# Optimization experiments

Measured on AMD Instinct MI355X. Metric: run time of the kernel, lower is better.

Reference implementation:

```python
import jax, jax.numpy as jnp
import numpy as np
import math

DN = ('NCHW', 'OIHW', 'NCHW')

def conv2d(x, w, b=None, pad=0):
    y = jax.lax.conv_general_dilated(x, w, (1, 1), [(pad, pad), (pad, pad)], dimension_numbers=DN)
    if b is not None:
        y = y + b[None, :, None, None]
    return y

def group_norm(x, weight, bias, groups=32, eps=1e-5):
    B, C, H, W = x.shape
    xg = x.reshape(B, groups, C // groups, H, W)
    mean = xg.mean(axis=(2, 3, 4), keepdims=True)
    var = xg.var(axis=(2, 3, 4), keepdims=True)
    xg = (xg - mean) * jax.lax.rsqrt(var + eps)
    return xg.reshape(B, C, H, W) * weight[None, :, None, None] + bias[None, :, None, None]

def swish(x):
    return x * jax.nn.sigmoid(x)

def setup_inputs() -> dict:
    key = jax.random.key(0)
    ks = jax.random.split(key, 20)
    B, C, H, W = 8, 192, 48, 48
    emb = 192
    n_div = 12
    Cq = C // n_div  # 16
    s = 0.02
    return {
        'x': jax.random.normal(ks[0], (B, C, H, W), jnp.float32),
        'xe': jax.random.normal(ks[1], (B, C, H, W), jnp.float32),
        'time_emb': jax.random.normal(ks[2], (B, emb), jnp.float32),
        'gn1_w': jnp.ones((C,), jnp.float32),
        'gn1_b': jnp.zeros((C,), jnp.float32),
        'conv1_w': jax.random.normal(ks[3], (C, C, 3, 3), jnp.float32) * s,
        'conv1_b': jnp.zeros((C,), jnp.float32),
        'aff_w': jax.random.normal(ks[4], (2 * C, emb), jnp.float32) * s,
        'aff_b': jnp.zeros((2 * C,), jnp.float32),
        'gn2_w': jnp.ones((C,), jnp.float32),
        'gn2_b': jnp.zeros((C,), jnp.float32),
        'conv2_w': jax.random.normal(ks[5], (C, C, 3, 3), jnp.float32) * s,
        'conv2_b': jnp.zeros((C,), jnp.float32),
        'q_w': jax.random.normal(ks[6], (Cq, C, 1, 1), jnp.float32) * s,
        'kv_w': jax.random.normal(ks[7], (2 * Cq, C, 1, 1), jnp.float32) * s,
        'out_w': jax.random.normal(ks[8], (C, Cq, 3, 3), jnp.float32) * s,
        'out_b': jnp.zeros((C,), jnp.float32),
    }

def reference(x, xe, time_emb, gn1_w, gn1_b, conv1_w, conv1_b, aff_w, aff_b,
              gn2_w, gn2_b, conv2_w, conv2_b, q_w, kv_w, out_w, out_b):
    B, C, H, W = x.shape
    n_head, n_div = 1, 12
    head_dim = C // (n_head * n_div)

    # ----- ResnetBlock -----
    h = conv2d(swish(group_norm(x, gn1_w, gn1_b)), conv1_w, conv1_b, pad=1)
    # FeatureWiseAffine (use_affine_level=True)
    gb = time_emb @ aff_w.T + aff_b          # [B, 2C]
    gamma, beta = jnp.split(gb, 2, axis=1)   # each [B, C]
    gb_sum = 0.5 * (gamma + beta)[:, :, None, None]
    h = h + gb_sum * h + gb_sum
    h = conv2d(swish(group_norm(h, gn2_w, gn2_b)), conv2_w, conv2_b, pad=1)
    xres = h + x  # res_conv is Identity (dim == dim_out)

    # ----- CrossAttention -----
    Ye, Xe = xe.shape[-2], xe.shape[-1]
    query = conv2d(xres, q_w).reshape(B, n_head, head_dim, H, W)
    kv = conv2d(xe, kv_w).reshape(B, n_head, head_dim * 2, Ye, Xe)
    key_, value = jnp.split(kv, 2, axis=2)
    scale = 1.0 / math.sqrt(C // n_div)
    attn = jnp.einsum('bnchw,bncyx->bnhwyx', query, key_) * scale
    attn = jax.nn.softmax(attn.reshape(B, n_head, H, W, -1), axis=-1)
    attn = attn.reshape(B, n_head, H, W, Ye, Xe)
    out = jnp.einsum('bnhwyx,bncyx->bnchw', attn, value)
    out = conv2d(out.reshape(B, C // n_div, H, W), out_w, out_b, pad=1)
    return out + xres
```

## Files before the change

kernel.cpp:

```cpp
#include <hip/hip_runtime.h>
#include <hip/hip_bf16.h>

#define NB 8
#define NC 192
#define NH 48
#define NW 48
#define NP 2304
#define NGROUPS 32
#define CPG 6
#define NEMB 192
#define NCQ 16

#define PH 50
#define PWS 52
#define ACT_T_ELEMS ((size_t)NB * PH * PWS * NC)
#define AOT_ELEMS   ((size_t)NB * PH * PWS * 16)

typedef __attribute__((ext_vector_type(4))) short s16x4;
typedef __attribute__((ext_vector_type(8))) short s16x8;
typedef __attribute__((ext_vector_type(4))) float f32x4;

static __device__ inline short f2bf(float v) {
  __hip_bfloat16 h = __float2bfloat16(v);
  return *(short*)&h;
}

__global__ __launch_bounds__(256) void wprep_kernel(const float* __restrict__ w,
                                                    short* __restrict__ wbuf) {
  int i = blockIdx.x * 256 + threadIdx.x;
  if (i >= 6 * 9 * 12 * 64 * 8) return;
  int j  = i & 7;
  int l  = (i >> 3) & 63;
  int cf = (i >> 9) % 12;
  int tk = (i >> 9) / 12;
  int t  = tk % 9;
  int kc = tk / 9;
  int co = cf * 16 + (l & 15);
  int ci = kc * 32 + (l >> 4) * 8 + j;
  wbuf[i] = f2bf(w[((size_t)co * NC + ci) * 9 + t]);
}

__global__ __launch_bounds__(256) void wprep_o_kernel(const float* __restrict__ w,
                                                      short* __restrict__ wbuf) {
  int i = blockIdx.x * 256 + threadIdx.x;
  if (i >= 9 * 12 * 64 * 8) return;
  int j  = i & 7;
  int l  = (i >> 3) & 63;
  int cf = (i >> 9) % 12;
  int t  = (i >> 9) / 12;
  int co = cf * 16 + (l & 15);
  int ci = (l >> 4) * 8 + j;
  wbuf[i] = (ci < 16) ? f2bf(w[((size_t)co * 16 + ci) * 9 + t]) : (short)0;
}

template <int NM>
__global__ __launch_bounds__(256) void wprep_a_kernel(const float* __restrict__ w,
                                                      short* __restrict__ aw, float scale) {
  int i = blockIdx.x * 256 + threadIdx.x;
  if (i >= 6 * NM * 64 * 8) return;
  int j = i & 7, l = (i >> 3) & 63, rest = i >> 9;
  int m = rest % NM, kc = rest / NM;
  int co = m * 16 + (l & 15);
  int ci = kc * 32 + (l >> 4) * 8 + j;
  aw[i] = f2bf(w[(size_t)co * NC + ci] * scale);
}

__global__ __launch_bounds__(256) void affine_kernel(const float* __restrict__ emb,
                                                     const float* __restrict__ aw,
                                                     const float* __restrict__ ab,
                                                     float* __restrict__ gbsum) {
  int i = blockIdx.x * 256 + threadIdx.x;
  if (i >= NB * NC) return;
  int b = i / NC;
  int c = i - b * NC;
  const float* e  = emb + b * NEMB;
  const float* w0 = aw + c * NEMB;
  const float* w1 = aw + (c + NC) * NEMB;
  float s = 0.f;
  for (int j = 0; j < NEMB; ++j) s += e[j] * (w0[j] + w1[j]);
  gbsum[i] = 0.5f * (s + ab[c] + ab[c + NC]);
}

__global__ __launch_bounds__(256) void halo_zero_kernel(short* __restrict__ actt) {
  int b = blockIdx.y;
  int i = blockIdx.x * 256 + threadIdx.x;
  if (i >= 9600) return;
  int c4 = i % 48;
  int r  = i / 48;
  size_t off;
  if (r < 52)       off = ((size_t)0 * PWS + r) * NC;
  else if (r < 104) off = ((size_t)49 * PWS + (r - 52)) * NC;
  else if (r < 152) off = ((size_t)(r - 104 + 1) * PWS + 0) * NC;
  else              off = ((size_t)(r - 152 + 1) * PWS + 49) * NC;
  *(s16x4*)(&actt[(size_t)b * PH * PWS * NC + off + c4 * 4]) = (s16x4){0, 0, 0, 0};
}

__global__ __launch_bounds__(256) void halo_zero16_kernel(short* __restrict__ aot) {
  int b = blockIdx.x;
  for (int i = threadIdx.x; i < 784; i += 256) {
    int c4  = i & 3;
    int pos = i >> 2;
    int r, col;
    if (pos < 50)       { r = 0;  col = pos; }
    else if (pos < 100) { r = 49; col = pos - 50; }
    else if (pos < 148) { r = pos - 100 + 1; col = 0; }
    else                { r = pos - 148 + 1; col = 49; }
    *(s16x4*)(&aot[(((size_t)b * PH + r) * PWS + col) * 16 + c4 * 4]) = (s16x4){0, 0, 0, 0};
  }
}

__global__ __launch_bounds__(192) void gn_stats_part_kernel(const float* __restrict__ in,
                                                            float* __restrict__ part) {
  int bg = blockIdx.x, seg = blockIdx.y;
  const float4* p = (const float4*)(in + (size_t)bg * (CPG * NP) + seg * 2304);
  float s = 0.f, s2 = 0.f;
  for (int i = threadIdx.x; i < 576; i += 192) {
    float4 v = p[i];
    s  += v.x + v.y + v.z + v.w;
    s2 += v.x * v.x + v.y * v.y + v.z * v.z + v.w * v.w;
  }
#pragma unroll
  for (int off = 32; off > 0; off >>= 1) {
    s  += __shfl_down(s, off);
    s2 += __shfl_down(s2, off);
  }
  __shared__ float red[6];
  int wave = threadIdx.x >> 6;
  if ((threadIdx.x & 63) == 0) { red[wave * 2] = s; red[wave * 2 + 1] = s2; }
  __syncthreads();
  if (threadIdx.x == 0) {
    part[(bg * 6 + seg) * 2]     = red[0] + red[2] + red[4];
    part[(bg * 6 + seg) * 2 + 1] = red[1] + red[3] + red[5];
  }
}

__global__ __launch_bounds__(256) void gn_stats_reduce_kernel(const float* __restrict__ part,
                                                              float* __restrict__ stats) {
  int bg = threadIdx.x;
  float S = 0.f, S2 = 0.f;
#pragma unroll
  for (int k = 0; k < 6; ++k) {
    S  += part[(bg * 6 + k) * 2];
    S2 += part[(bg * 6 + k) * 2 + 1];
  }
  const float invN = 1.f / (float)(CPG * NP);
  float mean = S * invN;
  float var  = S2 * invN - mean * mean;
  stats[bg * 2]     = mean;
  stats[bg * 2 + 1] = rsqrtf(var + 1e-5f);
}

__global__ __launch_bounds__(256) void gn_apply_t_kernel(const float* __restrict__ in,
                                                         const float* __restrict__ stats,
                                                         const float* __restrict__ gw,
                                                         const float* __restrict__ gb,
                                                         short* __restrict__ actt) {
  __shared__ float tile[48 * 193];
  int bh = blockIdx.x;
  int b = bh / NH;
  int h = bh - b * NH;
  int tid = threadIdx.x;
  for (int i = tid; i < 2304; i += 256) {
    int c = i / 12;
    int w = (i % 12) * 4;
    float4 v = *(const float4*)(in + (((size_t)b * NC + c) * NH + h) * NW + w);
    float mean = stats[(b * NGROUPS + c / CPG) * 2];
    float rstd = stats[(b * NGROUPS + c / CPG) * 2 + 1];
    float sc = rstd * gw[c];
    float sh = gb[c] - mean * sc;
    float y;
    y = v.x * sc + sh; tile[(w + 0) * 193 + c] = y / (1.f + __expf(-y));
    y = v.y * sc + sh; tile[(w + 1) * 193 + c] = y / (1.f + __expf(-y));
    y = v.z * sc + sh; tile[(w + 2) * 193 + c] = y / (1.f + __expf(-y));
    y = v.w * sc + sh; tile[(w + 3) * 193 + c] = y / (1.f + __expf(-y));
  }
  __syncthreads();
  short* dst = actt + (((size_t)b * PH + h + 1) * PWS + 1) * NC;
  for (int i = tid; i < 2304; i += 256) {
    int w  = i / 48;
    int c4 = (i - w * 48) * 4;
    s16x4 o;
    o.x = f2bf(tile[w * 193 + c4 + 0]);
    o.y = f2bf(tile[w * 193 + c4 + 1]);
    o.z = f2bf(tile[w * 193 + c4 + 2]);
    o.w = f2bf(tile[w * 193 + c4 + 3]);
    *(s16x4*)(dst + (size_t)w * NC + c4) = o;
  }
}

__global__ __launch_bounds__(256) void tconv_kernel(const float* __restrict__ in,
                                                    short* __restrict__ xT) {
  __shared__ float tile[48 * 193];
  int bh = blockIdx.x;
  int b = bh / NH;
  int h = bh - b * NH;
  int tid = threadIdx.x;
  for (int i = tid; i < 2304; i += 256) {
    int c = i / 12;
    int w = (i % 12) * 4;
    float4 v = *(const float4*)(in + (((size_t)b * NC + c) * NH + h) * NW + w);
    tile[(w + 0) * 193 + c] = v.x;
    tile[(w + 1) * 193 + c] = v.y;
    tile[(w + 2) * 193 + c] = v.z;
    tile[(w + 3) * 193 + c] = v.w;
  }
  __syncthreads();
  short* dst = xT + (size_t)(b * NP + h * NW) * NC;
  for (int i = tid; i < 2304; i += 256) {
    int w  = i / 48;
    int c4 = (i - w * 48) * 4;
    s16x4 o;
    o.x = f2bf(tile[w * 193 + c4 + 0]);
    o.y = f2bf(tile[w * 193 + c4 + 1]);
    o.z = f2bf(tile[w * 193 + c4 + 2]);
    o.w = f2bf(tile[w * 193 + c4 + 3]);
    *(s16x4*)(dst + (size_t)w * NC + c4) = o;
  }
}

template <int NM, bool ISKV>
__global__ __launch_bounds__(256) void qkv_mfma_kernel(const short* __restrict__ xT,
                                                       const short* __restrict__ aw,
                                                       short* __restrict__ KQ,
                                                       short* __restrict__ VTb) {
  int b    = blockIdx.y;
  int lane = threadIdx.x & 63;
  int wv   = threadIdx.x >> 6;
  int g    = lane >> 4, ql = lane & 15;
  int p    = blockIdx.x * 64 + wv * 16 + ql;

  f32x4 acc[NM];
#pragma unroll
  for (int m = 0; m < NM; ++m) acc[m] = (f32x4){0.f, 0.f, 0.f, 0.f};

  const short* bp = xT + ((size_t)b * NP + p) * NC + g * 8;
#pragma unroll
  for (int kc = 0; kc < 6; ++kc) {
    s16x8 bf = *(const s16x8*)(bp + kc * 32);
#pragma unroll
    for (int m = 0; m < NM; ++m) {
      s16x8 af = *(const s16x8*)(aw + ((size_t)(kc * NM + m) * 64 + lane) * 8);
      acc[m] = __builtin_amdgcn_mfma_f32_16x16x32_bf16(af, bf, acc[m], 0, 0, 0);
    }
  }
  s16x4 o0;
  o0.x = f2bf(acc[0][0]); o0.y = f2bf(acc[0][1]);
  o0.z = f2bf(acc[0][2]); o0.w = f2bf(acc[0][3]);
  *(s16x4*)(KQ + ((size_t)b * NP + p) * 32 + g * 4) = o0;
  *(s16x4*)(KQ + ((size_t)b * NP + p) * 32 + 16 + g * 4) = (s16x4){0, 0, 0, 0};
  if (ISKV) {
#pragma unroll
    for (int r = 0; r < 4; ++r)
      VTb[((size_t)b * 16 + g * 4 + r) * NP + p] = f2bf(acc[NM - 1][r]);
  }
}

template <bool AFFINE, bool RESID>
__global__ __launch_bounds__(256) void conv_mfma_kernel(const short* __restrict__ actt,
                                                        const short* __restrict__ wbuf,
                                                        const float* __restrict__ bias,
                                                        const float* __restrict__ gbsum,
                                                        const float* __restrict__ resid,
                                                        float* __restrict__ out) {
  __shared__ short S[4][50][40];
  int bs = blockIdx.x;
  int b = bs / 24;
  int strip = bs - b * 24;
  int coB = blockIdx.y;
  int h0 = strip * 2;
  int tid = threadIdx.x;
  int lane = tid & 63, wave = tid >> 6;
  int wy = wave >> 1, wx = wave & 1;
  int g8 = (lane >> 4) * 8;

  f32x4 acc[2][3];
#pragma unroll
  for (int m = 0; m < 2; ++m)
#pragma unroll
    for (int f = 0; f < 3; ++f) acc[m][f] = (f32x4){0.f, 0.f, 0.f, 0.f};

  const size_t actbase = ((size_t)b * PH + h0) * PWS * NC;

  for (int kc = 0; kc < 6; ++kc) {
    __syncthreads();
    for (int i = tid; i < 800; i += 256) {
      int ci8 = i & 3;
      int rc  = i >> 2;
      int col = rc % 50, r = rc / 50;
      const s16x8* src = (const s16x8*)(actt + actbase + ((size_t)r * PWS + col) * NC +
                                        kc * 32 + ci8 * 8);
      *(s16x8*)(&S[r][col][ci8 * 8]) = *src;
    }
    __syncthreads();
#pragma unroll
    for (int t = 0; t < 9; ++t) {
      int ky = t / 3, kx = t - ky * 3;
      const short* wp = wbuf + ((((size_t)kc * 9 + t) * 12 + (coB * 4 + wy * 2)) * 64 + lane) * 8;
      s16x8 a0 = *(const s16x8*)wp;
      s16x8 a1 = *(const s16x8*)(wp + 64 * 8);
      int row = wx + ky;
#pragma unroll
      for (int f = 0; f < 3; ++f) {
        int col = f * 16 + (lane & 15) + kx;
        s16x8 bf = *(const s16x8*)(&S[row][col][g8]);
        acc[0][f] = __builtin_amdgcn_mfma_f32_16x16x32_bf16(a0, bf, acc[0][f], 0, 0, 0);
        acc[1][f] = __builtin_amdgcn_mfma_f32_16x16x32_bf16(a1, bf, acc[1][f], 0, 0, 0);
      }
    }
  }
  int hout = h0 + wx;
#pragma unroll
  for (int m = 0; m < 2; ++m) {
    int co0 = coB * 64 + wy * 32 + m * 16;
#pragma unroll
    for (int r = 0; r < 4; ++r) {
      int co = co0 + (lane >> 4) * 4 + r;
      float bv = bias[co];
      float s = AFFINE ? gbsum[b * NC + co] : 0.f;
#pragma unroll
      for (int f = 0; f < 3; ++f) {
        int w = f * 16 + (lane & 15);
        size_t o = (((size_t)b * NC + co) * NH + hout) * NW + w;
        float v = acc[m][f][r] + bv;
        if (AFFINE) v = v * (1.f + s) + s;
        if (RESID) v += resid[o];
        out[o] = v;
      }
    }
  }
}

__global__ __launch_bounds__(256) void out_conv_mfma_kernel(const short* __restrict__ aot,
                                                            const short* __restrict__ wbuf,
                                                            const float* __restrict__ bias,
                                                            float* __restrict__ out) {
  __shared__ short S[4][50][40];
  int bs = blockIdx.x;
  int b = bs / 24;
  int strip = bs - b * 24;
  int coB = blockIdx.y;
  int h0 = strip * 2;
  int tid = threadIdx.x;
  int lane = tid & 63, wave = tid >> 6;
  int wy = wave >> 1, wx = wave & 1;
  int g8 = (lane >> 4) * 8;

  f32x4 acc[2][3];
#pragma unroll
  for (int m = 0; m < 2; ++m)
#pragma unroll
    for (int f = 0; f < 3; ++f) acc[m][f] = (f32x4){0.f, 0.f, 0.f, 0.f};

  const size_t base = ((size_t)b * PH + h0) * PWS * 16;
  for (int i = tid; i < 800; i += 256) {
    int ci8 = i & 3;
    int rc  = i >> 2;
    int col = rc % 50, r = rc / 50;
    s16x8 v = (s16x8){0, 0, 0, 0, 0, 0, 0, 0};
    if (ci8 < 2)
      v = *(const s16x8*)(aot + base + ((size_t)r * PWS + col) * 16 + ci8 * 8);
    *(s16x8*)(&S[r][col][ci8 * 8]) = v;
  }
  __syncthreads();
#pragma unroll
  for (int t = 0; t < 9; ++t) {
    int ky = t / 3, kx = t - ky * 3;
    const short* wp = wbuf + (((size_t)t * 12 + (coB * 4 + wy * 2)) * 64 + lane) * 8;
    s16x8 a0 = *(const s16x8*)wp;
    s16x8 a1 = *(const s16x8*)(wp + 64 * 8);
    int row = wx + ky;
#pragma unroll
    for (int f = 0; f < 3; ++f) {
      int col = f * 16 + (lane & 15) + kx;
      s16x8 bf = *(const s16x8*)(&S[row][col][g8]);
      acc[0][f] = __builtin_amdgcn_mfma_f32_16x16x32_bf16(a0, bf, acc[0][f], 0, 0, 0);
      acc[1][f] = __builtin_amdgcn_mfma_f32_16x16x32_bf16(a1, bf, acc[1][f], 0, 0, 0);
    }
  }
  int hout = h0 + wx;
#pragma unroll
  for (int m = 0; m < 2; ++m) {
    int co0 = coB * 64 + wy * 32 + m * 16;
#pragma unroll
    for (int r = 0; r < 4; ++r) {
      int co = co0 + (lane >> 4) * 4 + r;
      float bv = bias[co];
#pragma unroll
      for (int f = 0; f < 3; ++f) {
        int w = f * 16 + (lane & 15);
        size_t o = (((size_t)b * NC + co) * NH + hout) * NW + w;
        out[o] = acc[m][f][r] + bv + out[o];
      }
    }
  }
}

__global__ __launch_bounds__(1024) void attn_mfma_kernel(const short* __restrict__ Qb,
                                                         const short* __restrict__ Kb,
                                                         const short* __restrict__ VTb,
                                                         short* __restrict__ aot) {
  __shared__ float PM[4][4][64], PL[4][4][64];
  __shared__ f32x4 PA[4][4][64];
  int b    = blockIdx.y;
  int tid  = threadIdx.x;
  int lane = tid & 63;
  int w    = tid >> 6;
  int qg   = w & 3, ks = w >> 2;
  int q0   = blockIdx.x * 64 + qg * 16;
  int g    = lane >> 4;
  int ql   = lane & 15;

  s16x8 qfrag = *(const s16x8*)(Qb + ((size_t)b * NP + q0 + ql) * 32 + g * 8);

  int r0 = 8 * (ql >> 2) + (ql & 3);
  const short* Kbase = Kb + (size_t)b * NP * 32 + g * 8;
  const short* Vbase = VTb + ((size_t)b * 16 + ql) * NP;

  f32x4 acc = {0.f, 0.f, 0.f, 0.f};
  float m = -1e30f, l = 0.f;

  int kk = ks * 576;
  s16x8 kf0 = *(const s16x8*)(Kbase + (size_t)(kk + r0) * 32);
  s16x8 kf1 = *(const s16x8*)(Kbase + (size_t)(kk + r0 + 4) * 32);
  s16x8 vf  = *(const s16x8*)(Vbase + kk + g * 8);

  for (int step = 0; step < 18; ++step) {
    int kn = (step < 17) ? kk + 32 : ks * 576;
    s16x8 nk0 = *(const s16x8*)(Kbase + (size_t)(kn + r0) * 32);
    s16x8 nk1 = *(const s16x8*)(Kbase + (size_t)(kn + r0 + 4) * 32);
    s16x8 nv  = *(const s16x8*)(Vbase + kn + g * 8);

    f32x4 z = {0.f, 0.f, 0.f, 0.f};
    f32x4 s0 = __builtin_amdgcn_mfma_f32_16x16x32_bf16(kf0, qfrag, z, 0, 0, 0);
    f32x4 s1 = __builtin_amdgcn_mfma_f32_16x16x32_bf16(kf1, qfrag, z, 0, 0, 0);

    float tm = fmaxf(fmaxf(fmaxf(s0[0], s0[1]), fmaxf(s0[2], s0[3])),
                     fmaxf(fmaxf(s1[0], s1[1]), fmaxf(s1[2], s1[3])));
    if (!__all(tm <= m + 8.0f)) {
      tm = fmaxf(tm, __shfl_xor(tm, 16, 64));
      tm = fmaxf(tm, __shfl_xor(tm, 32, 64));
      float mn = fmaxf(m, tm);
      float corr = exp2f(m - mn);
      m = mn;
      l *= corr;
      acc[0] *= corr; acc[1] *= corr; acc[2] *= corr; acc[3] *= corr;
    }
    float p0 = exp2f(s0[0] - m), p1 = exp2f(s0[1] - m);
    float p2 = exp2f(s0[2] - m), p3 = exp2f(s0[3] - m);
    float p4 = exp2f(s1[0] - m), p5 = exp2f(s1[1] - m);
    float p6 = exp2f(s1[2] - m), p7 = exp2f(s1[3] - m);
    l += ((p0 + p1) + (p2 + p3)) + ((p4 + p5) + (p6 + p7));

    s16x8 pf;
    pf[0] = f2bf(p0); pf[1] = f2bf(p1); pf[2] = f2bf(p2); pf[3] = f2bf(p3);
    pf[4] = f2bf(p4); pf[5] = f2bf(p5); pf[6] = f2bf(p6); pf[7] = f2bf(p7);
    acc = __builtin_amdgcn_mfma_f32_16x16x32_bf16(vf, pf, acc, 0, 0, 0);

    kf0 = nk0; kf1 = nk1; vf = nv; kk = kn;
  }
  PM[ks][qg][lane] = m;
  PL[ks][qg][lane] = l;
  PA[ks][qg][lane] = acc;
  __syncthreads();
  if (ks == 0) {
    float M = PM[0][qg][lane];
#pragma unroll
    for (int k = 1; k < 4; ++k) M = fmaxf(M, PM[k][qg][lane]);
    float L = 0.f;
    f32x4 o = {0.f, 0.f, 0.f, 0.f};
#pragma unroll
    for (int k = 0; k < 4; ++k) {
      float c = exp2f(PM[k][qg][lane] - M);
      L += PL[k][qg][lane] * c;
      f32x4 a = PA[k][qg][lane];
      o[0] += a[0] * c; o[1] += a[1] * c; o[2] += a[2] * c; o[3] += a[3] * c;
    }
    L += __shfl_xor(L, 16, 64);
    L += __shfl_xor(L, 32, 64);
    float inv = 1.f / L;
    int q = q0 + ql;
    int h = q / NW, wcol = q - h * NW;
    s16x4 ov;
    ov.x = f2bf(o[0] * inv);
    ov.y = f2bf(o[1] * inv);
    ov.z = f2bf(o[2] * inv);
    ov.w = f2bf(o[3] * inv);
    *(s16x4*)(aot + (((size_t)b * PH + h + 1) * PWS + wcol + 1) * 16 + g * 4) = ov;
  }
}

extern "C" void kernel_launch(void* const* d_in, const int* in_sizes, int n_in,
                              void* d_out, int out_size, void* d_ws, size_t ws_size,
                              hipStream_t stream) {
  const float* x      = (const float*)d_in[0];
  const float* xe     = (const float*)d_in[1];
  const float* temb   = (const float*)d_in[2];
  const float* gn1w   = (const float*)d_in[3];
  const float* gn1b   = (const float*)d_in[4];
  const float* conv1w = (const float*)d_in[5];
  const float* conv1b = (const float*)d_in[6];
  const float* affw   = (const float*)d_in[7];
  const float* affb   = (const float*)d_in[8];
  const float* gn2w   = (const float*)d_in[9];
  const float* gn2b   = (const float*)d_in[10];
  const float* conv2w = (const float*)d_in[11];
  const float* conv2b = (const float*)d_in[12];
  const float* qw     = (const float*)d_in[13];
  const float* kvw    = (const float*)d_in[14];
  const float* outw   = (const float*)d_in[15];
  const float* outb   = (const float*)d_in[16];
  float* out = (float*)d_out;
  float* ws  = (float*)d_ws;

  const float SC = 0.36067376022224085f;

  float* gbsum  = ws;
  float* stats  = gbsum + NB * NC;
  float* gnpart = stats + 512;
  short* wbuf1  = (short*)(gnpart + 3072);
  short* wbuf2  = wbuf1 + (size_t)6 * 9 * 12 * 64 * 8;
  short* wbufo  = wbuf2 + (size_t)6 * 9 * 12 * 64 * 8;
  short* awq    = wbufo + (size_t)9 * 12 * 64 * 8;
  short* awkv   = awq + 3072;
  short* actt   = awkv + 6144;
  short* Qb     = actt + ACT_T_ELEMS;
  short* Kb     = Qb + (size_t)NB * NP * 32;
  short* VTb    = Kb + (size_t)NB * NP * 32;
  short* aot    = VTb + (size_t)NB * 16 * NP;
  short* xeT    = aot + AOT_ELEMS;
  short* xrT    = xeT + (size_t)NB * NP * NC;

  wprep_kernel<<<1296, 256, 0, stream>>>(conv1w, wbuf1);
  wprep_kernel<<<1296, 256, 0, stream>>>(conv2w, wbuf2);
  wprep_o_kernel<<<216, 256, 0, stream>>>(outw, wbufo);
  wprep_a_kernel<1><<<12, 256, 0, stream>>>(qw, awq, SC);
  wprep_a_kernel<2><<<24, 256, 0, stream>>>(kvw, awkv, 1.0f);
  affine_kernel<<<6, 256, 0, stream>>>(temb, affw, affb, gbsum);
  halo_zero_kernel<<<dim3(38, NB), 256, 0, stream>>>(actt);
  halo_zero16_kernel<<<NB, 256, 0, stream>>>(aot);

  tconv_kernel<<<NB * NH, 256, 0, stream>>>(xe, xeT);
  qkv_mfma_kernel<2, true><<<dim3(36, NB), 256, 0, stream>>>(xeT, awkv, Kb, VTb);

  gn_stats_part_kernel<<<dim3(NB * NGROUPS, 6), 192, 0, stream>>>(x, gnpart);
  gn_stats_reduce_kernel<<<1, 256, 0, stream>>>(gnpart, stats);
  gn_apply_t_kernel<<<NB * NH, 256, 0, stream>>>(x, stats, gn1w, gn1b, actt);
  conv_mfma_kernel<true, false><<<dim3(NB * 24, 3), 256, 0, stream>>>(
      actt, wbuf1, conv1b, gbsum, nullptr, out);
  gn_stats_part_kernel<<<dim3(NB * NGROUPS, 6), 192, 0, stream>>>(out, gnpart);
  gn_stats_reduce_kernel<<<1, 256, 0, stream>>>(gnpart, stats);
  gn_apply_t_kernel<<<NB * NH, 256, 0, stream>>>(out, stats, gn2w, gn2b, actt);
  conv_mfma_kernel<false, true><<<dim3(NB * 24, 3), 256, 0, stream>>>(
      actt, wbuf2, conv2b, nullptr, x, out);

  tconv_kernel<<<NB * NH, 256, 0, stream>>>(out, xrT);
  qkv_mfma_kernel<1, false><<<dim3(36, NB), 256, 0, stream>>>(xrT, awq, Qb, nullptr);
  attn_mfma_kernel<<<dim3(36, NB), 1024, 0, stream>>>(Qb, Kb, VTb, aot);
  out_conv_mfma_kernel<<<dim3(NB * 24, 3), 256, 0, stream>>>(aot, wbufo, outb, out);
}
```

Baseline: 275.8 us.

## Merge prep kernels, fuse transpose into QKV, inline GN reduce, double-buffer conv

```diff
diff --git a/kernel.cpp b/kernel.cpp
--- a/kernel.cpp
+++ b/kernel.cpp
@@ -25,87 +25,91 @@
   return *(short*)&h;
 }
 
-__global__ __launch_bounds__(256) void wprep_kernel(const float* __restrict__ w,
-                                                    short* __restrict__ wbuf) {
-  int i = blockIdx.x * 256 + threadIdx.x;
-  if (i >= 6 * 9 * 12 * 64 * 8) return;
-  int j  = i & 7;
-  int l  = (i >> 3) & 63;
-  int cf = (i >> 9) % 12;
-  int tk = (i >> 9) / 12;
-  int t  = tk % 9;
-  int kc = tk / 9;
-  int co = cf * 16 + (l & 15);
-  int ci = kc * 32 + (l >> 4) * 8 + j;
-  wbuf[i] = f2bf(w[((size_t)co * NC + ci) * 9 + t]);
-}
-
-__global__ __launch_bounds__(256) void wprep_o_kernel(const float* __restrict__ w,
-                                                      short* __restrict__ wbuf) {
-  int i = blockIdx.x * 256 + threadIdx.x;
-  if (i >= 9 * 12 * 64 * 8) return;
-  int j  = i & 7;
-  int l  = (i >> 3) & 63;
-  int cf = (i >> 9) % 12;
-  int t  = (i >> 9) / 12;
-  int co = cf * 16 + (l & 15);
-  int ci = (l >> 4) * 8 + j;
-  wbuf[i] = (ci < 16) ? f2bf(w[((size_t)co * 16 + ci) * 9 + t]) : (short)0;
-}
-
-template <int NM>
-__global__ __launch_bounds__(256) void wprep_a_kernel(const float* __restrict__ w,
-                                                      short* __restrict__ aw, float scale) {
-  int i = blockIdx.x * 256 + threadIdx.x;
-  if (i >= 6 * NM * 64 * 8) return;
-  int j = i & 7, l = (i >> 3) & 63, rest = i >> 9;
-  int m = rest % NM, kc = rest / NM;
-  int co = m * 16 + (l & 15);
-  int ci = kc * 32 + (l >> 4) * 8 + j;
-  aw[i] = f2bf(w[(size_t)co * NC + ci] * scale);
-}
-
-__global__ __launch_bounds__(256) void affine_kernel(const float* __restrict__ emb,
-                                                     const float* __restrict__ aw,
-                                                     const float* __restrict__ ab,
-                                                     float* __restrict__ gbsum) {
-  int i = blockIdx.x * 256 + threadIdx.x;
-  if (i >= NB * NC) return;
-  int b = i / NC;
-  int c = i - b * NC;
-  const float* e  = emb + b * NEMB;
-  const float* w0 = aw + c * NEMB;
-  const float* w1 = aw + (c + NC) * NEMB;
-  float s = 0.f;
-  for (int j = 0; j < NEMB; ++j) s += e[j] * (w0[j] + w1[j]);
-  gbsum[i] = 0.5f * (s + ab[c] + ab[c + NC]);
-}
-
-__global__ __launch_bounds__(256) void halo_zero_kernel(short* __restrict__ actt) {
-  int b = blockIdx.y;
-  int i = blockIdx.x * 256 + threadIdx.x;
-  if (i >= 9600) return;
-  int c4 = i % 48;
-  int r  = i / 48;
-  size_t off;
-  if (r < 52)       off = ((size_t)0 * PWS + r) * NC;
-  else if (r < 104) off = ((size_t)49 * PWS + (r - 52)) * NC;
-  else if (r < 152) off = ((size_t)(r - 104 + 1) * PWS + 0) * NC;
-  else              off = ((size_t)(r - 152 + 1) * PWS + 49) * NC;
-  *(s16x4*)(&actt[(size_t)b * PH * PWS * NC + off + c4 * 4]) = (s16x4){0, 0, 0, 0};
-}
-
-__global__ __launch_bounds__(256) void halo_zero16_kernel(short* __restrict__ aot) {
-  int b = blockIdx.x;
-  for (int i = threadIdx.x; i < 784; i += 256) {
-    int c4  = i & 3;
-    int pos = i >> 2;
-    int r, col;
-    if (pos < 50)       { r = 0;  col = pos; }
-    else if (pos < 100) { r = 49; col = pos - 50; }
-    else if (pos < 148) { r = pos - 100 + 1; col = 0; }
-    else                { r = pos - 148 + 1; col = 49; }
-    *(s16x4*)(&aot[(((size_t)b * PH + r) * PWS + col) * 16 + c4 * 4]) = (s16x4){0, 0, 0, 0};
+__global__ __launch_bounds__(256) void megaprep_kernel(
+    const float* __restrict__ conv1w, const float* __restrict__ conv2w,
+    const float* __restrict__ outw, const float* __restrict__ qw,
+    const float* __restrict__ kvw, const float* __restrict__ emb,
+    const float* __restrict__ affw, const float* __restrict__ affb,
+    short* __restrict__ wbuf1, short* __restrict__ wbuf2, short* __restrict__ wbufo,
+    short* __restrict__ awq, short* __restrict__ awkv,
+    float* __restrict__ gbsum, short* __restrict__ actt, short* __restrict__ aot) {
+  int bx = blockIdx.x;
+  int tid = threadIdx.x;
+  const float SC = 0.36067376022224085f;
+  if (bx < 2592) {
+    const float* w = (bx < 1296) ? conv1w : conv2w;
+    short* wb      = (bx < 1296) ? wbuf1 : wbuf2;
+    int i = ((bx < 1296) ? bx : bx - 1296) * 256 + tid;
+    int j  = i & 7;
+    int l  = (i >> 3) & 63;
+    int cf = (i >> 9) % 12;
+    int tk = (i >> 9) / 12;
+    int t  = tk % 9;
+    int kc = tk / 9;
+    int co = cf * 16 + (l & 15);
+    int ci = kc * 32 + (l >> 4) * 8 + j;
+    wb[i] = f2bf(w[((size_t)co * NC + ci) * 9 + t]);
+  } else if (bx < 2808) {
+    int i = (bx - 2592) * 256 + tid;
+    int j  = i & 7;
+    int l  = (i >> 3) & 63;
+    int cf = (i >> 9) % 12;
+    int t  = (i >> 9) / 12;
+    int co = cf * 16 + (l & 15);
+    int ci = (l >> 4) * 8 + j;
+    wbufo[i] = (ci < 16) ? f2bf(outw[((size_t)co * 16 + ci) * 9 + t]) : (short)0;
+  } else if (bx < 2820) {
+    int i = (bx - 2808) * 256 + tid;
+    int j = i & 7, l = (i >> 3) & 63, rest = i >> 9;
+    int kc = rest;
+    int co = (l & 15);
+    int ci = kc * 32 + (l >> 4) * 8 + j;
+    awq[i] = f2bf(qw[(size_t)co * NC + ci] * SC);
+  } else if (bx < 2844) {
+    int i = (bx - 2820) * 256 + tid;
+    int j = i & 7, l = (i >> 3) & 63, rest = i >> 9;
+    int m = rest % 2, kc = rest / 2;
+    int co = m * 16 + (l & 15);
+    int ci = kc * 32 + (l >> 4) * 8 + j;
+    awkv[i] = f2bf(kvw[(size_t)co * NC + ci]);
+  } else if (bx < 2850) {
+    int i = (bx - 2844) * 256 + tid;
+    if (i < NB * NC) {
+      int b = i / NC;
+      int c = i - b * NC;
+      const float* e  = emb + b * NEMB;
+      const float* w0 = affw + c * NEMB;
+      const float* w1 = affw + (c + NC) * NEMB;
+      float s = 0.f;
+      for (int j = 0; j < NEMB; ++j) s += e[j] * (w0[j] + w1[j]);
+      gbsum[i] = 0.5f * (s + affb[c] + affb[c + NC]);
+    }
+  } else if (bx < 3154) {
+    int rel = bx - 2850;
+    int b = rel / 38, xb = rel - b * 38;
+    int i = xb * 256 + tid;
+    if (i < 9600) {
+      int c4 = i % 48;
+      int r  = i / 48;
+      size_t off;
+      if (r < 52)       off = ((size_t)0 * PWS + r) * NC;
+      else if (r < 104) off = ((size_t)49 * PWS + (r - 52)) * NC;
+      else if (r < 152) off = ((size_t)(r - 104 + 1) * PWS + 0) * NC;
+      else              off = ((size_t)(r - 152 + 1) * PWS + 49) * NC;
+      *(s16x4*)(&actt[(size_t)b * PH * PWS * NC + off + c4 * 4]) = (s16x4){0, 0, 0, 0};
+    }
+  } else {
+    int b = bx - 3154;
+    for (int i = tid; i < 784; i += 256) {
+      int c4  = i & 3;
+      int pos = i >> 2;
+      int r, col;
+      if (pos < 50)       { r = 0;  col = pos; }
+      else if (pos < 100) { r = 49; col = pos - 50; }
+      else if (pos < 148) { r = pos - 100 + 1; col = 0; }
+      else                { r = pos - 148 + 1; col = 49; }
+      *(s16x4*)(&aot[(((size_t)b * PH + r) * PWS + col) * 16 + c4 * 4]) = (s16x4){0, 0, 0, 0};
+    }
   }
 }
 
@@ -134,40 +138,37 @@
   }
 }
 
-__global__ __launch_bounds__(256) void gn_stats_reduce_kernel(const float* __restrict__ part,
-                                                              float* __restrict__ stats) {
-  int bg = threadIdx.x;
-  float S = 0.f, S2 = 0.f;
-#pragma unroll
-  for (int k = 0; k < 6; ++k) {
-    S  += part[(bg * 6 + k) * 2];
-    S2 += part[(bg * 6 + k) * 2 + 1];
-  }
-  const float invN = 1.f / (float)(CPG * NP);
-  float mean = S * invN;
-  float var  = S2 * invN - mean * mean;
-  stats[bg * 2]     = mean;
-  stats[bg * 2 + 1] = rsqrtf(var + 1e-5f);
-}
-
 __global__ __launch_bounds__(256) void gn_apply_t_kernel(const float* __restrict__ in,
-                                                         const float* __restrict__ stats,
+                                                         const float* __restrict__ gnpart,
                                                          const float* __restrict__ gw,
                                                          const float* __restrict__ gb,
                                                          short* __restrict__ actt) {
   __shared__ float tile[48 * 193];
+  __shared__ float sst[32][2];
   int bh = blockIdx.x;
   int b = bh / NH;
   int h = bh - b * NH;
   int tid = threadIdx.x;
+  if (tid < 32) {
+    float S = 0.f, S2 = 0.f;
+#pragma unroll
+    for (int k = 0; k < 6; ++k) {
+      S  += gnpart[((b * 32 + tid) * 6 + k) * 2];
+      S2 += gnpart[((b * 32 + tid) * 6 + k) * 2 + 1];
+    }
+    const float invN = 1.f / (float)(CPG * NP);
+    float mean = S * invN;
+    float var  = S2 * invN - mean * mean;
+    sst[tid][0] = mean;
+    sst[tid][1] = rsqrtf(var + 1e-5f);
+  }
+  __syncthreads();
   for (int i = tid; i < 2304; i += 256) {
     int c = i / 12;
     int w = (i % 12) * 4;
     float4 v = *(const float4*)(in + (((size_t)b * NC + c) * NH + h) * NW + w);
-    float mean = stats[(b * NGROUPS + c / CPG) * 2];
-    float rstd = stats[(b * NGROUPS + c / CPG) * 2 + 1];
-    float sc = rstd * gw[c];
-    float sh = gb[c] - mean * sc;
+    float sc = sst[c / CPG][1] * gw[c];
+    float sh = gb[c] - sst[c / CPG][0] * sc;
     float y;
     y = v.x * sc + sh; tile[(w + 0) * 193 + c] = y / (1.f + __expf(-y));
     y = v.y * sc + sh; tile[(w + 1) * 193 + c] = y / (1.f + __expf(-y));
@@ -188,55 +189,41 @@
   }
 }
 
-__global__ __launch_bounds__(256) void tconv_kernel(const float* __restrict__ in,
-                                                    short* __restrict__ xT) {
+template <int NM, bool ISKV>
+__global__ __launch_bounds__(192) void qkv_fused_kernel(const float* __restrict__ X,
+                                                        const short* __restrict__ aw,
+                                                        short* __restrict__ KQ,
+                                                        short* __restrict__ VTb) {
   __shared__ float tile[48 * 193];
   int bh = blockIdx.x;
   int b = bh / NH;
   int h = bh - b * NH;
   int tid = threadIdx.x;
-  for (int i = tid; i < 2304; i += 256) {
+  for (int i = tid; i < 2304; i += 192) {
     int c = i / 12;
     int w = (i % 12) * 4;
-    float4 v = *(const float4*)(in + (((size_t)b * NC + c) * NH + h) * NW + w);
+    float4 v = *(const float4*)(X + (((size_t)b * NC + c) * NH + h) * NW + w);
     tile[(w + 0) * 193 + c] = v.x;
     tile[(w + 1) * 193 + c] = v.y;
     tile[(w + 2) * 193 + c] = v.z;
     tile[(w + 3) * 193 + c] = v.w;
   }
   __syncthreads();
-  short* dst = xT + (size_t)(b * NP + h * NW) * NC;
-  for (int i = tid; i < 2304; i += 256) {
-    int w  = i / 48;
-    int c4 = (i - w * 48) * 4;
-    s16x4 o;
-    o.x = f2bf(tile[w * 193 + c4 + 0]);
-    o.y = f2bf(tile[w * 193 + c4 + 1]);
-    o.z = f2bf(tile[w * 193 + c4 + 2]);
-    o.w = f2bf(tile[w * 193 + c4 + 3]);
-    *(s16x4*)(dst + (size_t)w * NC + c4) = o;
-  }
-}
-
-template <int NM, bool ISKV>
-__global__ __launch_bounds__(256) void qkv_mfma_kernel(const short* __restrict__ xT,
-                                                       const short* __restrict__ aw,
-                                                       short* __restrict__ KQ,
-                                                       short* __restrict__ VTb) {
-  int b    = blockIdx.y;
-  int lane = threadIdx.x & 63;
-  int wv   = threadIdx.x >> 6;
-  int g    = lane >> 4, ql = lane & 15;
-  int p    = blockIdx.x * 64 + wv * 16 + ql;
+  int lane = tid & 63, wv = tid >> 6;
+  int g = lane >> 4, ql = lane & 15;
+  int pxl = wv * 16 + ql;
+  int p   = h * NW + pxl;
 
   f32x4 acc[NM];
 #pragma unroll
   for (int m = 0; m < NM; ++m) acc[m] = (f32x4){0.f, 0.f, 0.f, 0.f};
 
-  const short* bp = xT + ((size_t)b * NP + p) * NC + g * 8;
+  const float* bp = &tile[pxl * 193 + g * 8];
 #pragma unroll
   for (int kc = 0; kc < 6; ++kc) {
-    s16x8 bf = *(const s16x8*)(bp + kc * 32);
+    s16x8 bf;
+#pragma unroll
+    for (int j = 0; j < 8; ++j) bf[j] = f2bf(bp[kc * 32 + j]);
 #pragma unroll
     for (int m = 0; m < NM; ++m) {
       s16x8 af = *(const s16x8*)(aw + ((size_t)(kc * NM + m) * 64 + lane) * 8);
@@ -262,7 +249,7 @@
                                                         const float* __restrict__ gbsum,
                                                         const float* __restrict__ resid,
                                                         float* __restrict__ out) {
-  __shared__ short S[4][50][40];
+  __shared__ short S[2][4][50][40];
   int bs = blockIdx.x;
   int b = bs / 24;
   int strip = bs - b * 24;
@@ -281,17 +268,22 @@
 
   const size_t actbase = ((size_t)b * PH + h0) * PWS * NC;
 
-  for (int kc = 0; kc < 6; ++kc) {
-    __syncthreads();
+  auto stage = [&](int buf, int kc) {
     for (int i = tid; i < 800; i += 256) {
       int ci8 = i & 3;
       int rc  = i >> 2;
       int col = rc % 50, r = rc / 50;
       const s16x8* src = (const s16x8*)(actt + actbase + ((size_t)r * PWS + col) * NC +
                                         kc * 32 + ci8 * 8);
-      *(s16x8*)(&S[r][col][ci8 * 8]) = *src;
-    }
-    __syncthreads();
+      *(s16x8*)(&S[buf][r][col][ci8 * 8]) = *src;
+    }
+  };
+
+  stage(0, 0);
+  __syncthreads();
+  for (int kc = 0; kc < 6; ++kc) {
+    if (kc < 5) stage((kc + 1) & 1, kc + 1);
+    int cur = kc & 1;
 #pragma unroll
     for (int t = 0; t < 9; ++t) {
       int ky = t / 3, kx = t - ky * 3;
@@ -302,11 +294,12 @@
 #pragma unroll
       for (int f = 0; f < 3; ++f) {
         int col = f * 16 + (lane & 15) + kx;
-        s16x8 bf = *(const s16x8*)(&S[row][col][g8]);
+        s16x8 bf = *(const s16x8*)(&S[cur][row][col][g8]);
         acc[0][f] = __builtin_amdgcn_mfma_f32_16x16x32_bf16(a0, bf, acc[0][f], 0, 0, 0);
         acc[1][f] = __builtin_amdgcn_mfma_f32_16x16x32_bf16(a1, bf, acc[1][f], 0, 0, 0);
       }
     }
+    __syncthreads();
   }
   int hout = h0 + wx;
 #pragma unroll
@@ -512,11 +505,8 @@
   float* out = (float*)d_out;
   float* ws  = (float*)d_ws;
 
-  const float SC = 0.36067376022224085f;
-
   float* gbsum  = ws;
-  float* stats  = gbsum + NB * NC;
-  float* gnpart = stats + 512;
+  float* gnpart = gbsum + NB * NC;
   short* wbuf1  = (short*)(gnpart + 3072);
   short* wbuf2  = wbuf1 + (size_t)6 * 9 * 12 * 64 * 8;
   short* wbufo  = wbuf2 + (size_t)6 * 9 * 12 * 64 * 8;
@@ -527,34 +517,22 @@
   short* Kb     = Qb + (size_t)NB * NP * 32;
   short* VTb    = Kb + (size_t)NB * NP * 32;
   short* aot    = VTb + (size_t)NB * 16 * NP;
-  short* xeT    = aot + AOT_ELEMS;
-  short* xrT    = xeT + (size_t)NB * NP * NC;
-
-  wprep_kernel<<<1296, 256, 0, stream>>>(conv1w, wbuf1);
-  wprep_kernel<<<1296, 256, 0, stream>>>(conv2w, wbuf2);
-  wprep_o_kernel<<<216, 256, 0, stream>>>(outw, wbufo);
-  wprep_a_kernel<1><<<12, 256, 0, stream>>>(qw, awq, SC);
-  wprep_a_kernel<2><<<24, 256, 0, stream>>>(kvw, awkv, 1.0f);
-  affine_kernel<<<6, 256, 0, stream>>>(temb, affw, affb, gbsum);
-  halo_zero_kernel<<<dim3(38, NB), 256, 0, stream>>>(actt);
-  halo_zero16_kernel<<<NB, 256, 0, stream>>>(aot);
-
-  tconv_kernel<<<NB * NH, 256, 0, stream>>>(xe, xeT);
-  qkv_mfma_kernel<2, true><<<dim3(36, NB), 256, 0, stream>>>(xeT, awkv, Kb, VTb);
+
+  megaprep_kernel<<<3162, 256, 0, stream>>>(conv1w, conv2w, outw, qw, kvw, temb,
+                                            affw, affb, wbuf1, wbuf2, wbufo, awq, awkv,
+                                            gbsum, actt, aot);
+  qkv_fused_kernel<2, true><<<NB * NH, 192, 0, stream>>>(xe, awkv, Kb, VTb);
 
   gn_stats_part_kernel<<<dim3(NB * NGROUPS, 6), 192, 0, stream>>>(x, gnpart);
-  gn_stats_reduce_kernel<<<1, 256, 0, stream>>>(gnpart, stats);
-  gn_apply_t_kernel<<<NB * NH, 256, 0, stream>>>(x, stats, gn1w, gn1b, actt);
+  gn_apply_t_kernel<<<NB * NH, 256, 0, stream>>>(x, gnpart, gn1w, gn1b, actt);
   conv_mfma_kernel<true, false><<<dim3(NB * 24, 3), 256, 0, stream>>>(
       actt, wbuf1, conv1b, gbsum, nullptr, out);
   gn_stats_part_kernel<<<dim3(NB * NGROUPS, 6), 192, 0, stream>>>(out, gnpart);
-  gn_stats_reduce_kernel<<<1, 256, 0, stream>>>(gnpart, stats);
-  gn_apply_t_kernel<<<NB * NH, 256, 0, stream>>>(out, stats, gn2w, gn2b, actt);
+  gn_apply_t_kernel<<<NB * NH, 256, 0, stream>>>(out, gnpart, gn2w, gn2b, actt);
   conv_mfma_kernel<false, true><<<dim3(NB * 24, 3), 256, 0, stream>>>(
       actt, wbuf2, conv2b, nullptr, x, out);
 
-  tconv_kernel<<<NB * NH, 256, 0, stream>>>(out, xrT);
-  qkv_mfma_kernel<1, false><<<dim3(36, NB), 256, 0, stream>>>(xrT, awq, Qb, nullptr);
+  qkv_fused_kernel<1, false><<<NB * NH, 192, 0, stream>>>(out, awq, Qb, nullptr);
   attn_mfma_kernel<<<dim3(36, NB), 1024, 0, stream>>>(Qb, Kb, VTb, aot);
   out_conv_mfma_kernel<<<dim3(NB * 24, 3), 256, 0, stream>>>(aot, wbufo, outb, out);
 }
```

After: 250.4 us. 1.1x faster.
